# Kernel tuning notes

Hardware: AMD Instinct MI355X
Metric: run time of the kernel (lower is better)

## Reference

```python
import jax, jax.numpy as jnp
import numpy as np

N = 25000
E = 400000
HIDDEN = 512
NH = 8
DH = HIDDEN // NH


def setup_inputs() -> dict:
    key = jax.random.key(0)
    ks = jax.random.split(key, 10)
    s = 1.0 / np.sqrt(HIDDEN)
    return {
        "h": jax.random.normal(ks[0], (N, HIDDEN), dtype=jnp.float32),
        "Wq": jax.random.normal(ks[1], (HIDDEN, HIDDEN), dtype=jnp.float32) * s,
        "bq": jnp.zeros((HIDDEN,), dtype=jnp.float32),
        "Wk": jax.random.normal(ks[2], (HIDDEN, HIDDEN), dtype=jnp.float32) * s,
        "bk": jnp.zeros((HIDDEN,), dtype=jnp.float32),
        "Wo": jax.random.normal(ks[3], (HIDDEN, HIDDEN), dtype=jnp.float32) * s,
        "bo": jnp.zeros((HIDDEN,), dtype=jnp.float32),
        "rows": jax.random.randint(ks[4], (E,), 0, N, dtype=jnp.int32),
        "cols": jax.random.randint(ks[5], (E,), 0, N, dtype=jnp.int32),
    }


def reference(h, Wq, bq, Wk, bk, Wo, bo, rows, cols):
    # Projections; reshape (N, dh, nh) exactly as the source does.
    q = (h @ Wq + bq).reshape(N, DH, NH)
    k = (h @ Wk + bk).reshape(N, DH, NH)
    v = k  # source bug kept faithfully: v = linear_k(h)

    # SDDMM: per-edge, per-head dot product (no 1/sqrt(dh) scaling in source).
    scores = jnp.einsum("edh,edh->eh", q[rows], k[cols])  # [E, NH]

    # Row-wise (source-node) segment softmax per head.
    m = jax.ops.segment_max(scores, rows, num_segments=N)       # [N, NH]
    ex = jnp.exp(scores - m[rows])                              # [E, NH]
    denom = jax.ops.segment_sum(ex, rows, num_segments=N)      # [N, NH]
    attn = ex / denom[rows]                                     # [E, NH]

    # SpMM: out[i] = sum_{j in nbr(i)} attn[ij] * v[j]
    msgs = attn[:, None, :] * v[cols]                           # [E, DH, NH]
    out = jax.ops.segment_sum(msgs, rows, num_segments=N)      # [N, DH, NH]

    return out.reshape(N, HIDDEN) @ Wo + bo
```

## Files before the change

kernel.cpp:

```cpp
#include <hip/hip_runtime.h>
#include <math.h>

typedef unsigned short u16;
typedef unsigned int u32;
typedef __attribute__((ext_vector_type(8))) _Float16 half8;
typedef __attribute__((ext_vector_type(2))) _Float16 half2v;
typedef __attribute__((ext_vector_type(8))) u16 ushort8;
typedef __attribute__((ext_vector_type(4))) float f32x4;

__device__ __forceinline__ u16 f2h(float f) {
    union { u16 u; _Float16 h; } c; c.h = (_Float16)f; return c.u;
}

#if __has_builtin(__builtin_amdgcn_fdot2)
#define FDOT2(a, b, c) __builtin_amdgcn_fdot2((a), (b), (c), false)
#else
#define FDOT2(a, b, c) fmaf((float)(a)[0], (float)(b)[0], \
                        fmaf((float)(a)[1], (float)(b)[1], (c)))
#endif

__device__ __forceinline__ void gload16(void* lds, const void* g) {
    __builtin_amdgcn_global_load_lds(
        (const __attribute__((address_space(1))) u32*)g,
        (__attribute__((address_space(3))) u32*)lds,
        16, 0, 0);
}

template <int OUTMODE>
__device__ __forceinline__ void gemm_body(
    const u16* A, const u16* Bt, const float* bias, void* Cout, int Mout,
    int m0, int n0, u16* As0, u16* As1, u16* Bs0, u16* Bs1)
{
    const int tid  = threadIdx.x;
    const int wave = tid >> 6;
    const int lane = tid & 63;
    const int wr = (wave >> 1) * 64;
    const int wc = (wave & 1) * 64;

    f32x4 acc[4][4];
#pragma unroll
    for (int i = 0; i < 4; ++i)
#pragma unroll
        for (int j = 0; j < 4; ++j) acc[i][j] = (f32x4){0.f, 0.f, 0.f, 0.f};

    const int srow  = lane >> 2;
    const int scolG = ((lane & 3) ^ ((srow >> 1) & 3)) * 8;
    const size_t gOffA = (size_t)(m0 + wave * 32 + srow) * 512 + scolG;
    const size_t gOffB = (size_t)(n0 + wave * 32 + srow) * 512 + scolG;
    const int lOff = wave * 1024 + srow * 32 + (lane & 3) * 8;

    const int fR = ((lane & 15) >> 1) & 3;
    const int paOff = (wr + (lane & 15)) * 32 + ((lane >> 4) ^ fR) * 8;
    const int pbOff = (wc + (lane & 15)) * 32 + ((lane >> 4) ^ fR) * 8;

    auto STAGE = [&](u16* sa, u16* sb, int ko) {
        gload16(sa + lOff,       A  + gOffA + ko);
        gload16(sa + lOff + 512, A  + gOffA + ko + 16 * 512);
        gload16(sb + lOff,       Bt + gOffB + ko);
        gload16(sb + lOff + 512, Bt + gOffB + ko + 16 * 512);
    };
    auto COMPUTE = [&](const u16* sa, const u16* sb) {
        half8 af[4], bf[4];
#pragma unroll
        for (int i = 0; i < 4; ++i) af[i] = *(const half8*)(sa + paOff + i * 512);
#pragma unroll
        for (int j = 0; j < 4; ++j) bf[j] = *(const half8*)(sb + pbOff + j * 512);
#pragma unroll
        for (int i = 0; i < 4; ++i)
#pragma unroll
            for (int j = 0; j < 4; ++j)
                acc[i][j] = __builtin_amdgcn_mfma_f32_16x16x32_f16(
                    af[i], bf[j], acc[i][j], 0, 0, 0);
    };

    STAGE(As0, Bs0, 0);
    __syncthreads();
#pragma unroll
    for (int kt = 0; kt < 16; kt += 2) {
        STAGE(As1, Bs1, (kt + 1) * 32);
        COMPUTE(As0, Bs0);
        __syncthreads();
        if (kt + 2 < 16) STAGE(As0, Bs0, (kt + 2) * 32);
        COMPUTE(As1, Bs1);
        __syncthreads();
    }

    const int ccol  = n0 + wc + (lane & 15);
    const int crow0 = m0 + wr + (lane >> 4) * 4;
#pragma unroll
    for (int j = 0; j < 4; ++j) {
        const float b = bias[ccol + j * 16];
#pragma unroll
        for (int i = 0; i < 4; ++i) {
#pragma unroll
            for (int r = 0; r < 4; ++r) {
                int row = crow0 + i * 16 + r;
                if (row < Mout) {
                    float v = acc[i][j][r] + b;
                    size_t off = (size_t)row * 512 + ccol + j * 16;
                    if (OUTMODE == 0) ((float*)Cout)[off] = v;
                    else              ((u16*)Cout)[off] = f2h(v);
                }
            }
        }
    }
}

__global__ __launch_bounds__(256) void gemm_qk(
    const u16* __restrict__ hh, const u16* __restrict__ Wqt,
    const u16* __restrict__ Wkt, const float* __restrict__ bqp,
    const float* __restrict__ bkp, u16* __restrict__ Qh,
    u16* __restrict__ Kb, int nPad,
    const int* __restrict__ rows, const int* __restrict__ cols,
    int* __restrict__ cursor, int* __restrict__ colc, int E, int nGemm)
{
    __shared__ __align__(16) u16 As0[4096], As1[4096], Bs0[4096], Bs1[4096];
    const int bid = blockIdx.x;
    if (bid >= nGemm) {
        int i = (bid - nGemm) * 256 + threadIdx.x;
        if (i < E) {
            int pos = atomicAdd(&cursor[rows[i]], 1);
            colc[pos] = cols[i];
        }
        return;
    }
    const int m = (bid >> 6) * 8 + (bid & 7);
    const int s = (bid >> 3) & 7;
    if (m >= nPad / 128) return;
    const int z = s >> 2;
    const int n = s & 3;

    const u16* Bt = z ? Wkt : Wqt;
    const float* bias = z ? bkp : bqp;
    u16* out = z ? Kb : Qh;
    gemm_body<1>(hh, Bt, bias, out, nPad, m * 128, n * 128,
                 As0, As1, Bs0, Bs1);
}

__global__ __launch_bounds__(256) void gemm_wo(
    const u16* __restrict__ A, const u16* __restrict__ Wot,
    const float* __restrict__ bo, float* __restrict__ C, int Mout, int nPad)
{
    const int bid = blockIdx.x;
    const int m = (bid >> 5) * 8 + (bid & 7);
    const int s = (bid >> 3) & 3;
    if (m >= nPad / 128) return;

    __shared__ __align__(16) u16 As0[4096], As1[4096], Bs0[4096], Bs1[4096];
    gemm_body<0>(A, Wot, bo, C, Mout, m * 128, s * 128,
                 As0, As1, Bs0, Bs1);
}

__global__ __launch_bounds__(256) void prep(
    const float* __restrict__ h, u16* __restrict__ hh, int nN,
    const int* __restrict__ rows, int* __restrict__ deg, int E,
    const float* __restrict__ Wq, const float* __restrict__ Wk,
    const float* __restrict__ Wo, const float* __restrict__ bq,
    const float* __restrict__ bk,
    u16* __restrict__ Wqt, u16* __restrict__ Wkt, u16* __restrict__ Wot,
    float* __restrict__ bqp, float* __restrict__ bkp,
    int nbH, int nbE)
{
    __shared__ float T[64][65];
    const int tid = threadIdx.x;
    const int b = blockIdx.x;

    if (b < nbH) {
        int t = b * 256 + tid;
        size_t e = (size_t)t * 8;
        int row = (int)(e >> 9);
        ushort8 o;
        if (row < nN) {
            f32x4 a = *(const f32x4*)(h + e);
            f32x4 bb = *(const f32x4*)(h + e + 4);
            float x[8] = {a.x, a.y, a.z, a.w, bb.x, bb.y, bb.z, bb.w};
#pragma unroll
            for (int i = 0; i < 8; ++i) o[i] = f2h(x[i]);
        } else {
            o = (ushort8){0,0,0,0,0,0,0,0};
        }
        *(ushort8*)(hh + e) = o;
        return;
    }
    if (b < nbH + nbE) {
        int i = (b - nbH) * 256 + tid;
        if (i < E) atomicAdd(&deg[rows[i]], 1);
        return;
    }
    int rem = b - nbH - nbE;
    const int z = rem >> 6;
    const int X = (rem & 7) * 64;
    const int Y = ((rem >> 3) & 7) * 64;

    const int r4 = tid >> 4;
    const int c4 = (tid & 15) * 4;
    if (z < 2) {
        const float* W = z ? Wk : Wq;
#pragma unroll
        for (int rr = 0; rr < 64; rr += 16) {
            f32x4 v = *(const f32x4*)(W + (size_t)(X + rr + r4) * 512 + Y + c4);
            T[rr + r4][c4 + 0] = v.x; T[rr + r4][c4 + 1] = v.y;
            T[rr + r4][c4 + 2] = v.z; T[rr + r4][c4 + 3] = v.w;
        }
    } else {
#pragma unroll
        for (int rr = 0; rr < 64; rr += 16) {
            int p2 = (rr + r4) * 8 + (X >> 6);
            f32x4 v = *(const f32x4*)(Wo + (size_t)p2 * 512 + Y + c4);
            T[rr + r4][c4 + 0] = v.x; T[rr + r4][c4 + 1] = v.y;
            T[rr + r4][c4 + 2] = v.z; T[rr + r4][c4 + 3] = v.w;
        }
    }
    __syncthreads();

    const int cc = tid >> 2;
    const int ks = (tid & 3) * 16;
    const int pc = Y + cc;
    const int ro = (z < 2) ? ((pc & 7) * 64 + (pc >> 3)) : pc;
    ushort8 h0, h1;
#pragma unroll
    for (int t = 0; t < 8; ++t) {
        h0[t] = f2h(T[ks + t][cc]);
        h1[t] = f2h(T[ks + 8 + t][cc]);
    }
    size_t o = (size_t)ro * 512 + X + ks;
    if (z == 0) {
        *(ushort8*)(Wqt + o) = h0; *(ushort8*)(Wqt + o + 8) = h1;
    } else if (z == 1) {
        *(ushort8*)(Wkt + o) = h0; *(ushort8*)(Wkt + o + 8) = h1;
    } else {
        *(ushort8*)(Wot + o) = h0; *(ushort8*)(Wot + o + 8) = h1;
        if (rem == 128) {
            for (int bi = tid; bi < 512; bi += 256) {
                int pp = (bi & 63) * 8 + (bi >> 6);
                bqp[bi] = bq[pp];
                bkp[bi] = bk[pp];
            }
        }
    }
}

#define SCAN_CHUNK 2048

__global__ __launch_bounds__(256) void scan_all(
    const int* __restrict__ deg, int* __restrict__ rowptr,
    int* __restrict__ cursor, int n, int nb)
{
    const int t = threadIdx.x;
    const int b = blockIdx.x;
    const int lane = t & 63, wv = t >> 6;
    __shared__ int ws[4], wsum[4];

    int pre = 0;
    for (int i = t; i < b * SCAN_CHUNK; i += 256) pre += deg[i];
#pragma unroll
    for (int off = 1; off < 64; off <<= 1) pre += __shfl_xor(pre, off, 64);
    if (lane == 0) ws[wv] = pre;
    __syncthreads();
    const int boff = ws[0] + ws[1] + ws[2] + ws[3];

    int base = b * SCAN_CHUNK + t * 8;
    int v[8];
    int s = 0;
#pragma unroll
    for (int i = 0; i < 8; ++i) {
        int g = base + i;
        v[i] = (g < n) ? deg[g] : 0;
        s += v[i];
    }
    int inc = s;
#pragma unroll
    for (int off = 1; off < 64; off <<= 1) {
        int x = __shfl_up(inc, off, 64);
        if (lane >= off) inc += x;
    }
    if (lane == 63) wsum[wv] = inc;
    __syncthreads();
    int excl = boff + inc - s;
    for (int i = 0; i < wv; ++i) excl += wsum[i];
#pragma unroll
    for (int i = 0; i < 8; ++i) {
        int g = base + i;
        if (g < n) { rowptr[g] = excl; cursor[g] = excl; }
        excl += v[i];
    }
    if (b == nb - 1 && t == 0)
        rowptr[n] = boff + wsum[0] + wsum[1] + wsum[2] + wsum[3];
}

__global__ __launch_bounds__(256) void node_agg(
    const u16* __restrict__ Qh, const u16* __restrict__ Kb,
    const int* __restrict__ rowptr, const int* __restrict__ colc,
    u16* __restrict__ aggb, int nN)
{
    int node = blockIdx.x * 4 + (threadIdx.x >> 6);
    int lane = threadIdx.x & 63;
    if (node >= nN) return;
    size_t base = (size_t)node * 512 + lane * 8;

    half8 qv = __builtin_nontemporal_load((const half8*)(Qh + base));
    half2v q2[4];
#pragma unroll
    for (int i = 0; i < 4; ++i) q2[i] = (half2v){qv[2 * i], qv[2 * i + 1]};

    int start = rowptr[node];
    int deg   = rowptr[node + 1] - start;
    const int* cp = colc + start;
    const size_t loff = (size_t)lane * 8;

    float m = -__builtin_inff();
    float den = 0.f;
    half2v acc2[4];
#pragma unroll
    for (int i = 0; i < 4; ++i) acc2[i] = (half2v){(_Float16)0.f, (_Float16)0.f};

    if (deg > 0) {
        const int dl = deg - 1;
        half8 k[8];
#pragma unroll
        for (int t = 0; t < 8; ++t) {
            int it = t < dl ? t : dl;
            k[t] = *(const half8*)(Kb + (size_t)cp[it] * 512 + loff);
        }
        for (int j = 0; j < deg; j += 8) {
            half8 nx[8];
#pragma unroll
            for (int t = 0; t < 8; ++t) {
                int it = j + 8 + t < dl ? j + 8 + t : dl;
                nx[t] = *(const half8*)(Kb + (size_t)cp[it] * 512 + loff);
            }

            float p[8];
#pragma unroll
            for (int t = 0; t < 8; ++t) {
                float s = 0.f;
#pragma unroll
                for (int i = 0; i < 4; ++i) {
                    half2v bb = (half2v){k[t][2 * i], k[t][2 * i + 1]};
                    s = FDOT2(q2[i], bb, s);
                }
                p[t] = s;
            }
#pragma unroll
            for (int off = 1; off < 8; off <<= 1) {
#pragma unroll
                for (int t = 0; t < 8; ++t) p[t] += __shfl_xor(p[t], off, 64);
            }

            float pm = p[0];
#pragma unroll
            for (int t = 1; t < 8; ++t) pm = fmaxf(pm, p[t]);
            if (__any(pm > m + 4.f)) {
                float mn = fmaxf(m, pm);
                float sc = __expf(m - mn);
                den *= sc;
                _Float16 sch = (_Float16)sc;
                half2v sc2 = {sch, sch};
#pragma unroll
                for (int i = 0; i < 4; ++i) acc2[i] *= sc2;
                m = mn;
            }
#pragma unroll
            for (int t = 0; t < 8; ++t) {
                float w = (j + t < deg) ? __expf(p[t] - m) : 0.f;
                den += w;
                _Float16 wh = (_Float16)w;
                half2v w2 = {wh, wh};
#pragma unroll
                for (int i = 0; i < 4; ++i) {
                    half2v bb = (half2v){k[t][2 * i], k[t][2 * i + 1]};
                    acc2[i] += w2 * bb;
                }
            }
#pragma unroll
            for (int t = 0; t < 8; ++t) k[t] = nx[t];
        }
    }

    float inv = (deg > 0) ? 1.f / den : 0.f;
    ushort8 o;
#pragma unroll
    for (int i = 0; i < 4; ++i) {
        o[2 * i]     = f2h((float)acc2[i][0] * inv);
        o[2 * i + 1] = f2h((float)acc2[i][1] * inv);
    }
    __builtin_nontemporal_store(o, (ushort8*)(aggb + base));
}

extern "C" void kernel_launch(void* const* d_in, const int* in_sizes, int n_in,
                              void* d_out, int out_size, void* d_ws, size_t ws_size,
                              hipStream_t stream)
{
    const float* h  = (const float*)d_in[0];
    const float* Wq = (const float*)d_in[1];
    const float* bq = (const float*)d_in[2];
    const float* Wk = (const float*)d_in[3];
    const float* bk = (const float*)d_in[4];
    const float* Wo = (const float*)d_in[5];
    const float* bo = (const float*)d_in[6];
    const int* rows = (const int*)d_in[7];
    const int* cols = (const int*)d_in[8];
    float* out = (float*)d_out;

    const int HID = 512;
    const int nN  = in_sizes[0] / HID;
    const int E   = in_sizes[7];
    const int nPad = (nN + 127) & ~127;
    const int nb = (nN + SCAN_CHUNK - 1) / SCAN_CHUNK;
    const int nbH = nPad * (HID / 8) / 256;
    const int nbE = (E + 255) / 256;
    const int nMt = nPad / 128;
    const int nGrp = (nMt + 7) / 8;
    const int nGemmQK = nGrp * 64;

    char* w = (char*)d_ws;
    u16* Kb  = (u16*)w;  w += (size_t)nPad * HID * 2;
    u16* hh  = (u16*)w;  w += (size_t)nPad * HID * 2;
    u16* Qh  = (u16*)w;  w += (size_t)nPad * HID * 2;
    u16* Wqt = (u16*)w;  w += 512 * 512 * 2;
    u16* Wkt = (u16*)w;  w += 512 * 512 * 2;
    u16* Wot = (u16*)w;  w += 512 * 512 * 2;
    float* bqp = (float*)w;  w += 512 * 4;
    float* bkp = (float*)w;  w += 512 * 4;
    int* rowptr = (int*)w;   w += (size_t)(nN + 1) * 4;
    int* cursor = (int*)w;   w += (size_t)nN * 4;
    int* deg    = (int*)w;   w += (size_t)nN * 4;
    int* bsum   = (int*)w;   w += 64 * 4;
    int* colc   = (int*)w;

    (void)hipMemsetAsync(deg, 0, (size_t)nN * sizeof(int), stream);

    prep<<<nbH + nbE + 192, 256, 0, stream>>>(
        h, hh, nN, rows, deg, E, Wq, Wk, Wo, bq, bk,
        Wqt, Wkt, Wot, bqp, bkp, nbH, nbE);

    scan_all<<<nb, 256, 0, stream>>>(deg, rowptr, cursor, nN, nb);

    gemm_qk<<<nGemmQK + nbE, 256, 0, stream>>>(
        hh, Wqt, Wkt, bqp, bkp, Qh, Kb, nPad,
        rows, cols, cursor, colc, E, nGemmQK);

    node_agg<<<(nN + 3) / 4, 256, 0, stream>>>(Qh, Kb, rowptr, colc, hh, nN);

    gemm_wo<<<nGrp * 32, 256, 0, stream>>>(hh, Wot, bo, out, nN, nPad);
}
```

Measured before the change: 226.2 us.

## Vectorize degree counting, nontemporal final stores, setprio in aggregation loop

The degree-count phase of prep now has each thread load four row indices with one vector load and issue four atomics, cutting that phase's block count by four. The output GEMM writes its fp32 results with nontemporal stores, while node_agg switches its aggregate store back to a normal cached store, since gemm_wo reads that data next. The compute section of node_agg's edge loop is wrapped in s_setprio to raise wave priority during math. These are small independent tweaks aimed at memory traffic and scheduling, and each is unlikely to matter much.

Result: no change. 223.4 us, median of 2 (-1.2%).

```diff
diff --git a/kernel.cpp b/kernel.cpp
--- a/kernel.cpp
+++ b/kernel.cpp
@@ -7,6 +7,7 @@
 typedef __attribute__((ext_vector_type(2))) _Float16 half2v;
 typedef __attribute__((ext_vector_type(8))) u16 ushort8;
 typedef __attribute__((ext_vector_type(4))) float f32x4;
+typedef __attribute__((ext_vector_type(4))) int int4v;
 
 __device__ __forceinline__ u16 f2h(float f) {
     union { u16 u; _Float16 h; } c; c.h = (_Float16)f; return c.u;
@@ -98,8 +99,9 @@
                 if (row < Mout) {
                     float v = acc[i][j][r] + b;
                     size_t off = (size_t)row * 512 + ccol + j * 16;
-                    if (OUTMODE == 0) ((float*)Cout)[off] = v;
-                    else              ((u16*)Cout)[off] = f2h(v);
+                    if (OUTMODE == 0)      ((float*)Cout)[off] = v;
+                    else if (OUTMODE == 1) ((u16*)Cout)[off] = f2h(v);
+                    else __builtin_nontemporal_store(v, (float*)Cout + off);
                 }
             }
         }
@@ -147,7 +149,7 @@
     if (m >= nPad / 128) return;
 
     __shared__ __align__(16) u16 As0[4096], As1[4096], Bs0[4096], Bs1[4096];
-    gemm_body<0>(A, Wot, bo, C, Mout, m * 128, s * 128,
+    gemm_body<2>(A, Wot, bo, C, Mout, m * 128, s * 128,
                  As0, As1, Bs0, Bs1);
 }
 
@@ -159,7 +161,7 @@
     const float* __restrict__ bk,
     u16* __restrict__ Wqt, u16* __restrict__ Wkt, u16* __restrict__ Wot,
     float* __restrict__ bqp, float* __restrict__ bkp,
-    int nbH, int nbE)
+    int nbH, int nbE4)
 {
     __shared__ float T[64][65];
     const int tid = threadIdx.x;
@@ -182,12 +184,20 @@
         *(ushort8*)(hh + e) = o;
         return;
     }
-    if (b < nbH + nbE) {
-        int i = (b - nbH) * 256 + tid;
-        if (i < E) atomicAdd(&deg[rows[i]], 1);
+    if (b < nbH + nbE4) {
+        int i = ((b - nbH) * 256 + tid) * 4;
+        if (i + 3 < E) {
+            int4v r = *(const int4v*)(rows + i);
+            atomicAdd(&deg[r.x], 1);
+            atomicAdd(&deg[r.y], 1);
+            atomicAdd(&deg[r.z], 1);
+            atomicAdd(&deg[r.w], 1);
+        } else {
+            for (int t = i; t < E; ++t) atomicAdd(&deg[rows[t]], 1);
+        }
         return;
     }
-    int rem = b - nbH - nbE;
+    int rem = b - nbH - nbE4;
     const int z = rem >> 6;
     const int X = (rem & 7) * 64;
     const int Y = ((rem >> 3) & 7) * 64;
@@ -330,6 +340,7 @@
                 nx[t] = *(const half8*)(Kb + (size_t)cp[it] * 512 + loff);
             }
 
+            __builtin_amdgcn_s_setprio(1);
             float p[8];
 #pragma unroll
             for (int t = 0; t < 8; ++t) {
@@ -372,6 +383,7 @@
                     acc2[i] += w2 * bb;
                 }
             }
+            __builtin_amdgcn_s_setprio(0);
 #pragma unroll
             for (int t = 0; t < 8; ++t) k[t] = nx[t];
         }
@@ -384,7 +396,7 @@
         o[2 * i]     = f2h((float)acc2[i][0] * inv);
         o[2 * i + 1] = f2h((float)acc2[i][1] * inv);
     }
-    __builtin_nontemporal_store(o, (ushort8*)(aggb + base));
+    *(ushort8*)(aggb + base) = o;
 }
 
 extern "C" void kernel_launch(void* const* d_in, const int* in_sizes, int n_in,
@@ -409,6 +421,7 @@
     const int nb = (nN + SCAN_CHUNK - 1) / SCAN_CHUNK;
     const int nbH = nPad * (HID / 8) / 256;
     const int nbE = (E + 255) / 256;
+    const int nbE4 = (E + 1023) / 1024;
     const int nMt = nPad / 128;
     const int nGrp = (nMt + 7) / 8;
     const int nGemmQK = nGrp * 64;
@@ -430,9 +443,9 @@
 
     (void)hipMemsetAsync(deg, 0, (size_t)nN * sizeof(int), stream);
 
-    prep<<<nbH + nbE + 192, 256, 0, stream>>>(
+    prep<<<nbH + nbE4 + 192, 256, 0, stream>>>(
         h, hh, nN, rows, deg, E, Wq, Wk, Wo, bq, bk,
-        Wqt, Wkt, Wot, bqp, bkp, nbH, nbE);
+        Wqt, Wkt, Wot, bqp, bkp, nbH, nbE4);
 
     scan_all<<<nb, 256, 0, stream>>>(deg, rowptr, cursor, nN, nb);
 
```
